# Optimization experiments

Hardware: AMD Instinct MI355X
Metric: run time of the kernel (lower is better)

The kernel has to match this reference:

```python
import jax, jax.numpy as jnp
import numpy as np

NSAMPLE = 16
BN_EPS = 1e-5


def setup_inputs() -> dict:
    key = jax.random.key(0)
    k1, k2, k3, k4, k5, k6 = jax.random.split(key, 6)
    B, N, Cin, Cout = 8, 8192, 64, 128
    xyz = jax.random.normal(k1, (B, N, 3), dtype=jnp.float32)
    feature = jax.random.normal(k2, (B, N, Cin), dtype=jnp.float32)
    W = jax.random.normal(k3, (Cin, Cout), dtype=jnp.float32) * 0.05
    b = jax.random.normal(k4, (Cout,), dtype=jnp.float32) * 0.01
    gamma = 1.0 + 0.1 * jax.random.normal(k5, (Cout,), dtype=jnp.float32)
    beta = 0.1 * jax.random.normal(k6, (Cout,), dtype=jnp.float32)
    return {"xyz": xyz, "feature": feature, "W": W, "b": b,
            "gamma": gamma, "beta": beta, "npoint": 2048}


def farthest_point_sample(xyz, npoint):
    # xyz: [B, N, 3] -> centroids: [B, npoint] int32
    B, N, _ = xyz.shape
    dist0 = jnp.full((B, N), 1e10, dtype=xyz.dtype)
    far0 = jnp.zeros((B,), dtype=jnp.int32)  # deterministic seed point (torch uses randint)

    def step(carry, _):
        distance, farthest = carry
        centroid = jnp.take_along_axis(xyz, farthest[:, None, None], axis=1)  # [B,1,3]
        d = jnp.sum((xyz - centroid) ** 2, axis=-1)  # [B,N]
        distance = jnp.minimum(distance, d)
        new_far = jnp.argmax(distance, axis=-1).astype(jnp.int32)
        return (distance, new_far), farthest

    (_, _), cents = jax.lax.scan(step, (dist0, far0), None, length=npoint)
    return cents.T  # [B, npoint]


def index_points(points, idx):
    # points: [B, N, C]; idx: [B, ...] -> [B, ..., C]
    B = points.shape[0]
    C = points.shape[-1]
    flat = idx.reshape(B, -1)
    out = jnp.take_along_axis(points, flat[..., None], axis=1)  # [B, M, C]
    return out.reshape(idx.shape + (C,))


def knn_point(nsample, xyz, new_xyz):
    # squared distances [B, npoint, N], then nsample smallest
    sqr = (-2.0 * jnp.einsum('bmc,bnc->bmn', new_xyz, xyz)
           + jnp.sum(new_xyz ** 2, -1)[..., None]
           + jnp.sum(xyz ** 2, -1)[:, None, :])
    _, idx = jax.lax.top_k(-sqr, nsample)
    return idx  # [B, npoint, nsample]


def reference(xyz, feature, W, b, gamma, beta, npoint):
    B = xyz.shape[0]
    new_xyz_idx = farthest_point_sample(xyz, npoint)          # [B, npoint]
    new_xyz = index_points(xyz, new_xyz_idx)                  # [B, npoint, 3]
    idx = knn_point(NSAMPLE, xyz, new_xyz)                    # [B, npoint, K]
    grouped_feature = index_points(feature, idx)              # [B, npoint, K, Cin]

    # pointwise MLP: Linear -> BatchNorm (batch stats, per out-channel) -> ReLU
    h = jnp.einsum('bnkc,cd->bnkd', grouped_feature, W) + b   # [B, npoint, K, Cout]
    mean = jnp.mean(h, axis=(0, 1, 2))
    var = jnp.mean((h - mean) ** 2, axis=(0, 1, 2))           # biased, as torch BN
    h = gamma * (h - mean) * jax.lax.rsqrt(var + BN_EPS) + beta
    h = jax.nn.relu(h)

    new_feature = jnp.max(h, axis=2)                          # [B, npoint, Cout]
    return new_xyz, new_feature
```

## Files before the change

### kernel.cpp

```cpp
#include <hip/hip_runtime.h>

typedef unsigned long long u64;
typedef unsigned int u32;

constexpr int BATCH  = 8;
constexpr int NPTS   = 8192;
constexpr int CIN    = 64;
constexpr int COUT   = 128;
constexpr int NPOINT = 2048;
constexpr int KNN    = 16;

__global__ __launch_bounds__(256) void pp_kernel(const float* __restrict__ xyz,
                                                 float* __restrict__ pp) {
  int i = blockIdx.x * 256 + threadIdx.x;
  float x = xyz[i * 3 + 0], y = xyz[i * 3 + 1], z = xyz[i * 3 + 2];
  pp[i] = __fadd_rn(__fadd_rn(__fmul_rn(x, x), __fmul_rn(y, y)), __fmul_rn(z, z));
}

constexpr int FPS_T = 256;
constexpr int FPS_PPT = NPTS / FPS_T;

__global__ __launch_bounds__(256) void fps_kernel(const float* __restrict__ xyz,
                                                  float* __restrict__ out_xyz) {
  __shared__ float sX[NPTS], sY[NPTS], sZ[NPTS];
  __shared__ u64 sKey[2][4];
  const int b = blockIdx.x;
  const int t = threadIdx.x;
  const int lane = t & 63;
  const int wv = t >> 6;
  const float* xb = xyz + (size_t)b * NPTS * 3;
  float px[FPS_PPT], py[FPS_PPT], pz[FPS_PPT], pd[FPS_PPT];
#pragma unroll
  for (int j = 0; j < FPS_PPT; ++j) {
    int p = t + j * FPS_T;
    float x = xb[p * 3 + 0], y = xb[p * 3 + 1], z = xb[p * 3 + 2];
    px[j] = x; py[j] = y; pz[j] = z; pd[j] = 1e10f;
    sX[p] = x; sY[p] = y; sZ[p] = z;
  }
  float cx = xb[0], cy = xb[1], cz = xb[2];
  float* outx = out_xyz + (size_t)b * NPOINT * 3;
  __syncthreads();
  for (int it = 0; it < NPOINT; ++it) {
    if (t == 0) {
      outx[it * 3 + 0] = cx; outx[it * 3 + 1] = cy; outx[it * 3 + 2] = cz;
    }
    float bd = -1.0f; int bj = 0;
#pragma unroll
    for (int j = 0; j < FPS_PPT; ++j) {
      float dx = __fsub_rn(px[j], cx);
      float dy = __fsub_rn(py[j], cy);
      float dz = __fsub_rn(pz[j], cz);
      float d = __fadd_rn(__fadd_rn(__fmul_rn(dx, dx), __fmul_rn(dy, dy)),
                          __fmul_rn(dz, dz));
      float nd = fminf(pd[j], d);
      pd[j] = nd;
      if (nd > bd) { bd = nd; bj = j; }
    }
    const int bi0 = t + bj * FPS_T;
    u64 key = ((u64)__float_as_uint(bd) << 32) | (u32)(8191 - bi0);
#pragma unroll
    for (int off = 32; off >= 1; off >>= 1) {
      u64 ok = __shfl_xor(key, off);
      if (ok > key) key = ok;
    }
    const int par = it & 1;
    if (lane == 0) sKey[par][wv] = key;
    __syncthreads();
    u64 k0 = sKey[par][0];
    u64 k1 = sKey[par][1];
    u64 k2 = sKey[par][2];
    u64 k3 = sKey[par][3];
    if (k1 > k0) k0 = k1;
    if (k3 > k2) k2 = k3;
    if (k2 > k0) k0 = k2;
    const int bi = 8191 - (int)(u32)(k0 & 0xFFFFFFFFu);
    cx = sX[bi]; cy = sY[bi]; cz = sZ[bi];
  }
}

__global__ __launch_bounds__(512) void knn_kernel(const float* __restrict__ xyz,
                                                  const float* __restrict__ pp,
                                                  const float* __restrict__ new_xyz,
                                                  int* __restrict__ knn_idx) {
  __shared__ u64 smem[8192];
  const int tid = threadIdx.x;
  const int lane = tid & 63;
  const int wv = __builtin_amdgcn_readfirstlane(tid >> 6);
  const int bid = blockIdx.x;
  const int b = bid >> 5;
  const int qbase = (bid & 31) * 64;
  const int q = qbase + lane;
  const float* xb = xyz + (size_t)b * NPTS * 3;
  const float* ppb = pp + (size_t)b * NPTS;
  const float* nq = new_xyz + ((size_t)b * NPOINT + q) * 3;
  float qx = nq[0], qy = nq[1], qz = nq[2];
  float qq = __fadd_rn(__fadd_rn(__fmul_rn(qx, qx), __fmul_rn(qy, qy)),
                       __fmul_rn(qz, qz));

  u64 L[16];
#pragma unroll
  for (int s = 0; s < 16; ++s) L[s] = 0xFF800000FFFFFFFFULL;
  float cmax = __uint_as_float(0x7F800000u);
  int cnt = 0;

  auto flushfn = [&]() {
#pragma unroll
    for (int e = 0; e < 8; ++e) {
      if (e < cnt) {
        u64 key = smem[tid * 9 + e];
        if (key < L[15]) {
#pragma unroll
          for (int s = 15; s >= 1; --s)
            L[s] = (key < L[s - 1]) ? L[s - 1] : ((key < L[s]) ? key : L[s]);
          L[0] = (key < L[0]) ? key : L[0];
        }
      }
    }
    cnt = 0;
    u32 hb = (u32)(L[15] >> 32);
    hb ^= (hb >= 0x80000000u) ? 0x80000000u : 0xFFFFFFFFu;
    cmax = __uint_as_float(hb);
  };

  const int base = wv * 1024;
#pragma unroll 8
  for (int i = 0; i < 1024; ++i) {
    const int pidx = base + i;
    float ptx = xb[pidx * 3 + 0], pty = xb[pidx * 3 + 1], ptz = xb[pidx * 3 + 2];
    float pv = ppb[pidx];
    float dot = __fadd_rn(__fadd_rn(__fmul_rn(qx, ptx), __fmul_rn(qy, pty)),
                          __fmul_rn(qz, ptz));
    float d = __fadd_rn(__fadd_rn(__fmul_rn(-2.0f, dot), qq), pv);
    if (d <= cmax) {
      u32 xb32 = __float_as_uint(d);
      xb32 ^= ((int)xb32 < 0) ? 0xFFFFFFFFu : 0x80000000u;
      smem[tid * 9 + cnt] = ((u64)xb32 << 32) | (u32)pidx;
      ++cnt;
    }
    if (__any(cnt >= 8)) flushfn();
  }
  flushfn();
  __syncthreads();
#pragma unroll
  for (int s = 0; s < 16; ++s) smem[tid * 16 + s] = L[s];
  __syncthreads();
  if (tid < 64) {
    u64 h[8]; int pos[8];
#pragma unroll
    for (int w = 0; w < 8; ++w) { h[w] = smem[(w * 64 + tid) * 16]; pos[w] = 1; }
    int outv[16];
#pragma unroll
    for (int r = 0; r < 16; ++r) {
      u64 mv = h[0]; int mw = 0;
#pragma unroll
      for (int w = 1; w < 8; ++w) {
        if (h[w] < mv) { mv = h[w]; mw = w; }
      }
      outv[r] = (int)(mv & 0xFFFFFFFFULL);
#pragma unroll
      for (int w = 0; w < 8; ++w) {
        if (w == mw) {
          h[w] = (pos[w] < 16) ? smem[(w * 64 + tid) * 16 + pos[w]]
                               : 0xFFFFFFFFFFFFFFFFULL;
          pos[w]++;
        }
      }
    }
    int* dst = knn_idx + ((size_t)b * NPOINT + qbase + tid) * KNN;
#pragma unroll
    for (int r = 0; r < 16; r += 4)
      *(int4*)(dst + r) = make_int4(outv[r], outv[r + 1], outv[r + 2], outv[r + 3]);
  }
}

__global__ __launch_bounds__(256) void stats_kernel(const float* __restrict__ feature,
                                                    const float* __restrict__ Wm,
                                                    const float* __restrict__ bias,
                                                    const int* __restrict__ knn_idx,
                                                    double* __restrict__ stats) {
  __shared__ float s_part[256];
  const int tid = threadIdx.x;
  const int lane = tid & 63;
  const int wv = tid >> 6;
  const int tbase = blockIdx.x * 256 + tid;
  for (int chunk = 0; chunk < 4; ++chunk) {
    const int c0 = chunk * 32;
    float V[64];
#pragma unroll
    for (int j = 0; j < 64; ++j) V[j] = 0.f;
    for (int rr = 0; rr < 4; ++rr) {
      const int row = tbase + rr * 65536;
      const int bb = row >> 15;
      const int nbr = knn_idx[row];
      const float4* fp = (const float4*)(feature + ((size_t)bb * NPTS + nbr) * CIN);
      float acc[32];
#pragma unroll
      for (int j = 0; j < 32; ++j) acc[j] = bias[c0 + j];
      for (int cb = 0; cb < 8; ++cb) {
        float4 fa = fp[cb * 2 + 0], fb2 = fp[cb * 2 + 1];
        float fr[8] = {fa.x, fa.y, fa.z, fa.w, fb2.x, fb2.y, fb2.z, fb2.w};
#pragma unroll
        for (int cc = 0; cc < 8; ++cc) {
          const int c = cb * 8 + cc;
#pragma unroll
          for (int j = 0; j < 32; ++j)
            acc[j] = fmaf(fr[cc], Wm[c * COUT + c0 + j], acc[j]);
        }
      }
#pragma unroll
      for (int j = 0; j < 32; ++j) {
        V[j] += acc[j];
        V[32 + j] = fmaf(acc[j], acc[j], V[32 + j]);
      }
    }
#pragma unroll
    for (int o = 32; o >= 1; o >>= 1) {
      const bool hi = (lane & o) != 0;
#pragma unroll
      for (int j = 0; j < o; ++j) {
        float keep = hi ? V[o + j] : V[j];
        float send = hi ? V[j] : V[o + j];
        V[j] = keep + __shfl_xor(send, o);
      }
    }
    s_part[wv * 64 + lane] = V[0];
    __syncthreads();
    if (tid < 64) {
      float tot = s_part[tid] + s_part[64 + tid] + s_part[128 + tid] + s_part[192 + tid];
      int addr = (tid < 32) ? (c0 + tid) : (COUT + c0 + (tid - 32));
      atomicAdd(stats + addr, (double)tot);
    }
    __syncthreads();
  }
}

__global__ __launch_bounds__(256) void apply_kernel(const float* __restrict__ feature,
                                                    const float* __restrict__ Wm,
                                                    const float* __restrict__ bias,
                                                    const float* __restrict__ gamma,
                                                    const float* __restrict__ beta,
                                                    const int* __restrict__ knn_idx,
                                                    const double* __restrict__ stats,
                                                    float* __restrict__ out_feat) {
  __shared__ float s_sc[COUT], s_sh[COUT];
  const int tid = threadIdx.x;
  if (tid < COUT) {
    const double inv_n = 1.0 / (double)(BATCH * NPOINT * KNN);
    double mean = stats[tid] * inv_n;
    double var = stats[COUT + tid] * inv_n - mean * mean;
    double s = (double)gamma[tid] / sqrt(var + 1e-5);
    s_sc[tid] = (float)s;
    s_sh[tid] = (float)((double)beta[tid] - mean * s);
  }
  __syncthreads();
  const int k = tid & 15;
  const int qg = blockIdx.x * 16 + (tid >> 4);
  const int bb = qg >> 11;
  const int nbr = knn_idx[qg * KNN + k];
  const float4* fp = (const float4*)(feature + ((size_t)bb * NPTS + nbr) * CIN);
  float* outp = out_feat + (size_t)qg * COUT;
  for (int chunk = 0; chunk < 4; ++chunk) {
    const int c0 = chunk * 32;
    float acc[32];
#pragma unroll
    for (int j = 0; j < 32; ++j) acc[j] = bias[c0 + j];
    for (int cb = 0; cb < 8; ++cb) {
      float4 fa = fp[cb * 2 + 0], fb2 = fp[cb * 2 + 1];
      float fr[8] = {fa.x, fa.y, fa.z, fa.w, fb2.x, fb2.y, fb2.z, fb2.w};
#pragma unroll
      for (int cc = 0; cc < 8; ++cc) {
        const int c = cb * 8 + cc;
#pragma unroll
        for (int j = 0; j < 32; ++j)
          acc[j] = fmaf(fr[cc], Wm[c * COUT + c0 + j], acc[j]);
      }
    }
#pragma unroll
    for (int j = 0; j < 32; ++j) {
      float n = fmaxf(fmaf(acc[j], s_sc[c0 + j], s_sh[c0 + j]), 0.0f);
#pragma unroll
      for (int off = 8; off >= 1; off >>= 1)
        n = fmaxf(n, __shfl_xor(n, off));
      acc[j] = n;
    }
    if (k == 0) {
#pragma unroll
      for (int j = 0; j < 32; j += 4)
        *(float4*)(outp + c0 + j) = make_float4(acc[j], acc[j + 1], acc[j + 2], acc[j + 3]);
    }
  }
}

extern "C" void kernel_launch(void* const* d_in, const int* in_sizes, int n_in,
                              void* d_out, int out_size, void* d_ws, size_t ws_size,
                              hipStream_t stream) {
  (void)in_sizes; (void)n_in; (void)out_size; (void)ws_size;
  const float* xyz = (const float*)d_in[0];
  const float* feature = (const float*)d_in[1];
  const float* Wm = (const float*)d_in[2];
  const float* bias = (const float*)d_in[3];
  const float* gamma = (const float*)d_in[4];
  const float* beta = (const float*)d_in[5];

  float* out_xyz = (float*)d_out;
  float* out_feat = (float*)d_out + (size_t)BATCH * NPOINT * 3;

  int* knn_idx = (int*)d_ws;
  double* stats = (double*)((char*)d_ws + (1 << 20));
  float* pp = (float*)((char*)d_ws + (1 << 20) + 4096);

  pp_kernel<<<dim3(256), dim3(256), 0, stream>>>(xyz, pp);
  fps_kernel<<<dim3(BATCH), dim3(FPS_T), 0, stream>>>(xyz, out_xyz);
  knn_kernel<<<dim3(256), dim3(512), 0, stream>>>(xyz, pp, out_xyz, knn_idx);
  hipMemsetAsync(stats, 0, 2 * COUT * sizeof(double), stream);
  stats_kernel<<<dim3(256), dim3(256), 0, stream>>>(feature, Wm, bias, knn_idx, stats);
  apply_kernel<<<dim3(1024), dim3(256), 0, stream>>>(feature, Wm, bias, gamma, beta,
                                                     knn_idx, stats, out_feat);
}
```

Before: 2.607 ms.

## Use packed float2 math, DPP wave reduction, and float4 LDS in FPS

The farthest-point-sampling inner loop now processes point pairs with two-wide float vectors, so the compiler can emit packed FP32 instructions. The 64-bit shuffle-xor wave argmax is replaced by DPP row shifts and row broadcasts on split hi/lo 32-bit keys, with the result read from lane 63. Centroid coordinates are fetched from a single float4 LDS array instead of three separate arrays. The aim is to shorten the serial per-iteration latency of the 2048-step FPS loop, which runs on only 8 blocks; contraction is disabled to keep the distance rounding bit-exact.

```diff
diff --git a/kernel.cpp b/kernel.cpp
--- a/kernel.cpp
+++ b/kernel.cpp
@@ -2,6 +2,7 @@
 
 typedef unsigned long long u64;
 typedef unsigned int u32;
+typedef float f32x2 __attribute__((ext_vector_type(2)));
 
 constexpr int BATCH  = 8;
 constexpr int NPTS   = 8192;
@@ -18,24 +19,42 @@
 }
 
 constexpr int FPS_T = 256;
-constexpr int FPS_PPT = NPTS / FPS_T;
+constexpr int FPS_PAIRS = NPTS / FPS_T / 2;
+
+#define DPP_LVL(CTRL)                                                          \
+  {                                                                            \
+    u32 hi_o = (u32)__builtin_amdgcn_update_dpp((int)khi, (int)khi, (CTRL),    \
+                                                0xf, 0xf, false);              \
+    u32 lo_o = (u32)__builtin_amdgcn_update_dpp((int)klo, (int)klo, (CTRL),    \
+                                                0xf, 0xf, false);              \
+    bool gt = (hi_o > khi) || ((hi_o == khi) && (lo_o > klo));                 \
+    khi = gt ? hi_o : khi;                                                     \
+    klo = gt ? lo_o : klo;                                                     \
+  }
 
 __global__ __launch_bounds__(256) void fps_kernel(const float* __restrict__ xyz,
                                                   float* __restrict__ out_xyz) {
-  __shared__ float sX[NPTS], sY[NPTS], sZ[NPTS];
+#pragma clang fp contract(off)
+  __shared__ float4 sP[NPTS];
   __shared__ u64 sKey[2][4];
   const int b = blockIdx.x;
   const int t = threadIdx.x;
   const int lane = t & 63;
   const int wv = t >> 6;
   const float* xb = xyz + (size_t)b * NPTS * 3;
-  float px[FPS_PPT], py[FPS_PPT], pz[FPS_PPT], pd[FPS_PPT];
-#pragma unroll
-  for (int j = 0; j < FPS_PPT; ++j) {
-    int p = t + j * FPS_T;
-    float x = xb[p * 3 + 0], y = xb[p * 3 + 1], z = xb[p * 3 + 2];
-    px[j] = x; py[j] = y; pz[j] = z; pd[j] = 1e10f;
-    sX[p] = x; sY[p] = y; sZ[p] = z;
+  f32x2 px2[FPS_PAIRS], py2[FPS_PAIRS], pz2[FPS_PAIRS], pd2[FPS_PAIRS];
+#pragma unroll
+  for (int jp = 0; jp < FPS_PAIRS; ++jp) {
+    int p0 = t + (2 * jp) * FPS_T;
+    int p1 = t + (2 * jp + 1) * FPS_T;
+    float x0 = xb[p0 * 3 + 0], y0 = xb[p0 * 3 + 1], z0 = xb[p0 * 3 + 2];
+    float x1 = xb[p1 * 3 + 0], y1 = xb[p1 * 3 + 1], z1 = xb[p1 * 3 + 2];
+    px2[jp] = (f32x2){x0, x1};
+    py2[jp] = (f32x2){y0, y1};
+    pz2[jp] = (f32x2){z0, z1};
+    pd2[jp] = (f32x2){1e10f, 1e10f};
+    sP[p0] = make_float4(x0, y0, z0, 0.f);
+    sP[p1] = make_float4(x1, y1, z1, 0.f);
   }
   float cx = xb[0], cy = xb[1], cz = xb[2];
   float* outx = out_xyz + (size_t)b * NPOINT * 3;
@@ -44,27 +63,31 @@
     if (t == 0) {
       outx[it * 3 + 0] = cx; outx[it * 3 + 1] = cy; outx[it * 3 + 2] = cz;
     }
-    float bd = -1.0f; int bj = 0;
-#pragma unroll
-    for (int j = 0; j < FPS_PPT; ++j) {
-      float dx = __fsub_rn(px[j], cx);
-      float dy = __fsub_rn(py[j], cy);
-      float dz = __fsub_rn(pz[j], cz);
-      float d = __fadd_rn(__fadd_rn(__fmul_rn(dx, dx), __fmul_rn(dy, dy)),
-                          __fmul_rn(dz, dz));
-      float nd = fminf(pd[j], d);
-      pd[j] = nd;
-      if (nd > bd) { bd = nd; bj = j; }
+    const f32x2 cx2 = {cx, cx}, cy2 = {cy, cy}, cz2 = {cz, cz};
+    float bd = -1.0f;
+    int bj = 0;
+#pragma unroll
+    for (int jp = 0; jp < FPS_PAIRS; ++jp) {
+      f32x2 dx = px2[jp] - cx2;
+      f32x2 dy = py2[jp] - cy2;
+      f32x2 dz = pz2[jp] - cz2;
+      f32x2 d = (dx * dx + dy * dy) + dz * dz;
+      f32x2 nd = __builtin_elementwise_min(pd2[jp], d);
+      pd2[jp] = nd;
+      if (nd.x > bd) { bd = nd.x; bj = 2 * jp; }
+      if (nd.y > bd) { bd = nd.y; bj = 2 * jp + 1; }
     }
     const int bi0 = t + bj * FPS_T;
-    u64 key = ((u64)__float_as_uint(bd) << 32) | (u32)(8191 - bi0);
-#pragma unroll
-    for (int off = 32; off >= 1; off >>= 1) {
-      u64 ok = __shfl_xor(key, off);
-      if (ok > key) key = ok;
-    }
+    u32 khi = __float_as_uint(bd);
+    u32 klo = (u32)(8191 - bi0);
+    DPP_LVL(0x111)
+    DPP_LVL(0x112)
+    DPP_LVL(0x114)
+    DPP_LVL(0x118)
+    DPP_LVL(0x142)
+    DPP_LVL(0x143)
     const int par = it & 1;
-    if (lane == 0) sKey[par][wv] = key;
+    if (lane == 63) sKey[par][wv] = ((u64)khi << 32) | klo;
     __syncthreads();
     u64 k0 = sKey[par][0];
     u64 k1 = sKey[par][1];
@@ -74,7 +97,8 @@
     if (k3 > k2) k2 = k3;
     if (k2 > k0) k0 = k2;
     const int bi = 8191 - (int)(u32)(k0 & 0xFFFFFFFFu);
-    cx = sX[bi]; cy = sY[bi]; cz = sZ[bi];
+    float4 c4 = sP[bi];
+    cx = c4.x; cy = c4.y; cz = c4.z;
   }
 }
 
@@ -312,7 +336,7 @@
   pp_kernel<<<dim3(256), dim3(256), 0, stream>>>(xyz, pp);
   fps_kernel<<<dim3(BATCH), dim3(FPS_T), 0, stream>>>(xyz, out_xyz);
   knn_kernel<<<dim3(256), dim3(512), 0, stream>>>(xyz, pp, out_xyz, knn_idx);
-  hipMemsetAsync(stats, 0, 2 * COUT * sizeof(double), stream);
+  (void)hipMemsetAsync(stats, 0, 2 * COUT * sizeof(double), stream);
   stats_kernel<<<dim3(256), dim3(256), 0, stream>>>(feature, Wm, bias, knn_idx, stats);
   apply_kernel<<<dim3(1024), dim3(256), 0, stream>>>(feature, Wm, bias, gamma, beta,
                                                      knn_idx, stats, out_feat);
```

Measured after the change: 2.406 ms. -7.7%, faster.
